# Kernel tuning notes

Hardware: AMD Instinct MI355X
Metric: run time of the kernel (lower is better)

## Reference

```python
import jax, jax.numpy as jnp
import numpy as np

N_SRC0, N_FTRS, N_HID, N_CLS = 200000, 128, 1500, 64
E0, E1 = 1600000, 500000
RES0, RES1 = 50000, 10000


def sage_conv(x, src, tgt, res_size, W_root, W_neigh, b):
    # mean aggregation of neighbor (source) features onto the first res_size target nodes
    msg = x[src]                                              # [E, F] gather
    summed = jax.ops.segment_sum(msg, tgt, num_segments=res_size)   # [res, F]
    cnt = jax.ops.segment_sum(jnp.ones((src.shape[0],), x.dtype), tgt, num_segments=res_size)
    mean = summed / jnp.maximum(cnt, 1.0)[:, None]
    return x[:res_size] @ W_root + mean @ W_neigh + b


def setup_inputs() -> dict:
    key = jax.random.key(0)
    ks = jax.random.split(key, 12)
    x = jax.random.normal(ks[0], (N_SRC0, N_FTRS), dtype=jnp.float32)
    edge_src0 = jax.random.randint(ks[1], (E0,), 0, N_SRC0)
    edge_tgt0 = jax.random.randint(ks[2], (E0,), 0, RES0)
    edge_src1 = jax.random.randint(ks[3], (E1,), 0, RES0)
    edge_tgt1 = jax.random.randint(ks[4], (E1,), 0, RES1)
    s1 = 1.0 / np.sqrt(N_FTRS)
    s2 = 1.0 / np.sqrt(N_HID)
    W1_root = jax.random.uniform(ks[5], (N_FTRS, N_HID), jnp.float32, -s1, s1)
    W1_neigh = jax.random.uniform(ks[6], (N_FTRS, N_HID), jnp.float32, -s1, s1)
    b1 = jax.random.uniform(ks[7], (N_HID,), jnp.float32, -s1, s1)
    W2_root = jax.random.uniform(ks[8], (N_HID, N_CLS), jnp.float32, -s2, s2)
    W2_neigh = jax.random.uniform(ks[9], (N_HID, N_CLS), jnp.float32, -s2, s2)
    b2 = jax.random.uniform(ks[10], (N_CLS,), jnp.float32, -s2, s2)
    return {
        "x": x,
        "W1_root": W1_root, "W1_neigh": W1_neigh, "b1": b1,
        "W2_root": W2_root, "W2_neigh": W2_neigh, "b2": b2,
        "edge_src0": edge_src0, "edge_tgt0": edge_tgt0,
        "edge_src1": edge_src1, "edge_tgt1": edge_tgt1,
        "res0": RES0, "res1": RES1,
    }


def reference(x, W1_root, W1_neigh, b1, W2_root, W2_neigh, b2,
              edge_src0, edge_tgt0, edge_src1, edge_tgt1, res0, res1):
    h = sage_conv(x, edge_src0, edge_tgt0, res0, W1_root, W1_neigh, b1)  # [res0, H]
    h = jax.nn.relu(h)
    # dropout p=0.5 is identity in eval mode
    out = sage_conv(h, edge_src1, edge_tgt1, res1, W2_root, W2_neigh, b2)  # [res1, C]
    return jax.nn.log_softmax(out, axis=1)
```

## Files before the change

### kernel.cpp

```cpp
#include <hip/hip_runtime.h>
#include <hip/hip_bf16.h>
#include <cstdint>
#include <cstddef>

#define NSRC   200000
#define NF     128
#define NHID   1500
#define NHIDP  1536
#define NCLS   64
#define E0N    1600000
#define E1N    500000
#define RES0   50000
#define RES1   10000

#define CH     4096
#define NCH0   ((E0N + CH - 1) / CH)
#define NCH1   ((E1N + CH - 1) / CH)
#define NB0    ((RES0 + 255) / 256)
#define NB1    ((RES1 + 255) / 256)

typedef __bf16 bf16x8 __attribute__((ext_vector_type(8)));
typedef float  f32x4  __attribute__((ext_vector_type(4)));
typedef unsigned short u16x8 __attribute__((ext_vector_type(8)));
typedef unsigned int u32;
typedef unsigned long long u64;

__device__ __forceinline__ unsigned short f2bf(float f) {
    union { float f; unsigned u; } v; v.f = f;
    unsigned r = v.u + 0x7fffu + ((v.u >> 16) & 1u);
    return (unsigned short)(r >> 16);
}

__device__ __forceinline__ void lds_dma16(const void* g, void* lds) {
    __builtin_amdgcn_global_load_lds(
        (const __attribute__((address_space(1))) unsigned int*)g,
        (__attribute__((address_space(3))) unsigned int*)lds, 16, 0, 0);
}

__global__ void prep_kernel(const float* __restrict__ W1r, const float* __restrict__ W1n,
                            const float* __restrict__ b1,
                            const float* __restrict__ W2r, const float* __restrict__ W2n,
                            unsigned short* __restrict__ WcatT,
                            unsigned short* __restrict__ W2catT,
                            float* __restrict__ b1e) {
    int id = blockIdx.x * 256 + threadIdx.x;
    if (id < 256 * NHIDP) {
        int n = id >> 8, k = id & 255;
        float v = 0.f;
        if (n < NHID) v = (k < NF) ? W1r[k * NHID + n] : W1n[(k - NF) * NHID + n];
        WcatT[n * 256 + k] = f2bf(v);
    } else {
        int id2 = id - 256 * NHIDP;
        if (id2 < 128 * NHIDP) {
            int n = id2 / NHIDP, k = id2 % NHIDP;
            float v = 0.f;
            if (k < NHID) v = (n < 64) ? W2n[k * 64 + n] : W2r[k * 64 + (n - 64)];
            W2catT[n * NHIDP + k] = f2bf(v);
        } else {
            int c = id2 - 128 * NHIDP;
            if (c < NHIDP) b1e[c] = (c < NHID) ? b1[c] : 0.f;
        }
    }
}

__global__ __launch_bounds__(256) void copyx_kernel(const float* __restrict__ x,
                                                    unsigned short* __restrict__ xbf) {
    size_t i = ((size_t)blockIdx.x * 256 + threadIdx.x) * 8;
    const float4* s = (const float4*)(x + i);
    float4 a = s[0], b = s[1];
    u16x8 o;
    o[0] = f2bf(a.x); o[1] = f2bf(a.y); o[2] = f2bf(a.z); o[3] = f2bf(a.w);
    o[4] = f2bf(b.x); o[5] = f2bf(b.y); o[6] = f2bf(b.z); o[7] = f2bf(b.w);
    *(u16x8*)(xbf + i) = o;
}

__global__ __launch_bounds__(256) void p1a_kernel(const int* __restrict__ tgt, int n,
                                                  int nb, u32* __restrict__ H) {
    __shared__ u32 lhist[256];
    int c = blockIdx.x, tid = threadIdx.x;
    lhist[tid] = 0;
    __syncthreads();
#pragma unroll
    for (int it = 0; it < CH / 256; ++it) {
        int i = c * CH + it * 256 + tid;
        if (i < n) atomicAdd(&lhist[((u32)tgt[i]) >> 8], 1u);
    }
    __syncthreads();
    if (tid < nb) H[c * nb + tid] = lhist[tid];
}

__global__ __launch_bounds__(512) void bscan_kernel(const u32* __restrict__ H,
                                                    int nch, int nb,
                                                    u32* __restrict__ base_rel,
                                                    u32* __restrict__ Bsum) {
    __shared__ u32 part[512];
    int b = blockIdx.x, t = threadIdx.x;
    part[t] = (t < nch) ? H[t * nb + b] : 0u;
    __syncthreads();
    for (int d = 1; d < 512; d <<= 1) {
        u32 v = part[t];
        u32 add = (t >= d) ? part[t - d] : 0u;
        __syncthreads();
        part[t] = v + add;
        __syncthreads();
    }
    if (t < nch) base_rel[t * nb + b] = (t == 0) ? 0u : part[t - 1];
    if (t == 0) Bsum[b] = part[nch - 1];
}

__global__ __launch_bounds__(256) void boff_kernel(const u32* __restrict__ Bsum1,
                                                   u32* __restrict__ boff1, int nb1,
                                                   const u32* __restrict__ Bsum2,
                                                   u32* __restrict__ boff2, int nb2) {
    const u32* B = blockIdx.x ? Bsum2 : Bsum1;
    u32* O = blockIdx.x ? boff2 : boff1;
    int nb = blockIdx.x ? nb2 : nb1;
    __shared__ u32 part[256];
    int t = threadIdx.x;
    part[t] = (t < nb) ? B[t] : 0u;
    __syncthreads();
    for (int d = 1; d < 256; d <<= 1) {
        u32 v = part[t];
        u32 add = (t >= d) ? part[t - d] : 0u;
        __syncthreads();
        part[t] = v + add;
        __syncthreads();
    }
    if (t < nb) O[t] = (t == 0) ? 0u : part[t - 1];
}

__global__ __launch_bounds__(256) void p1b_kernel(const int* __restrict__ src,
                                                  const int* __restrict__ tgt, int n,
                                                  int nb, const u32* __restrict__ base_rel,
                                                  const u32* __restrict__ boff,
                                                  u64* __restrict__ bucketed) {
    __shared__ u32 lcur[256];
    __shared__ u32 lbase[256];
    int c = blockIdx.x, tid = threadIdx.x;
    lcur[tid] = 0;
    if (tid < nb) lbase[tid] = base_rel[c * nb + tid] + boff[tid];
    __syncthreads();
#pragma unroll
    for (int it = 0; it < CH / 256; ++it) {
        int i = c * CH + it * 256 + tid;
        if (i < n) {
            u32 t = (u32)tgt[i];
            u32 s = (u32)src[i];
            u32 b = t >> 8;
            u32 r = atomicAdd(&lcur[b], 1u);
            bucketed[lbase[b] + r] = ((u64)t << 32) | (u64)s;
        }
    }
}

__global__ __launch_bounds__(1024) void p2_kernel(const u64* __restrict__ bucketed,
                                                  const u32* __restrict__ boff,
                                                  int nb, int res, int etot,
                                                  int* __restrict__ csr,
                                                  u32* __restrict__ off_out,
                                                  u32* __restrict__ cnt_out) {
    __shared__ u32 lhist[256];
    __shared__ u32 part[256];
    __shared__ u32 cur[256];
    int b = blockIdx.x, tid = threadIdx.x;
    u32 start = boff[b];
    u32 end = (b == nb - 1) ? (u32)etot : boff[b + 1];
    u32 count = end - start;
    if (tid < 256) lhist[tid] = 0;
    __syncthreads();
    for (u32 i = tid; i < count; i += 1024) {
        u32 t = (u32)(bucketed[start + i] >> 32);
        atomicAdd(&lhist[t & 255u], 1u);
    }
    __syncthreads();
    if (tid < 256) part[tid] = lhist[tid];
    __syncthreads();
    for (int d = 1; d < 256; d <<= 1) {
        u32 v = (tid < 256) ? part[tid] : 0u;
        u32 add = (tid >= d && tid < 256) ? part[tid - d] : 0u;
        __syncthreads();
        if (tid < 256) part[tid] = v + add;
        __syncthreads();
    }
    if (tid < 256) {
        u32 excl = (tid == 0) ? 0u : part[tid - 1];
        cur[tid] = excl;
        int tg = (b << 8) + tid;
        if (tg < res) {
            off_out[tg] = start + excl;
            cnt_out[tg] = lhist[tid];
        }
    }
    __syncthreads();
    for (u32 i = tid; i < count; i += 1024) {
        u64 pr = bucketed[start + i];
        u32 lt = ((u32)(pr >> 32)) & 255u;
        u32 r = atomicAdd(&cur[lt], 1u);
        csr[start + r] = (int)(u32)pr;
    }
}

__global__ __launch_bounds__(256) void agg1_csr_kernel(
        const u32* __restrict__ xb32, const int* __restrict__ csr,
        const u32* __restrict__ off, const u32* __restrict__ cnt,
        u32* __restrict__ mean1_32) {
    int row = blockIdx.x * 4 + (threadIdx.x >> 6);
    int lane = threadIdx.x & 63;
    if (row >= RES0) return;
    u32 base = off[row], deg = cnt[row];
    float x0 = 0.f, y0 = 0.f, x1 = 0.f, y1 = 0.f;
    float x2 = 0.f, y2 = 0.f, x3 = 0.f, y3 = 0.f;
    u32 e = 0;
    for (; e + 4 <= deg; e += 4) {
        int s0 = csr[base + e], s1 = csr[base + e + 1];
        int s2 = csr[base + e + 2], s3 = csr[base + e + 3];
        u32 w0 = xb32[(size_t)s0 * 64 + lane];
        u32 w1 = xb32[(size_t)s1 * 64 + lane];
        u32 w2 = xb32[(size_t)s2 * 64 + lane];
        u32 w3 = xb32[(size_t)s3 * 64 + lane];
        union { u32 u; float f; } a, b;
        a.u = w0 << 16; b.u = w0 & 0xffff0000u; x0 += a.f; y0 += b.f;
        a.u = w1 << 16; b.u = w1 & 0xffff0000u; x1 += a.f; y1 += b.f;
        a.u = w2 << 16; b.u = w2 & 0xffff0000u; x2 += a.f; y2 += b.f;
        a.u = w3 << 16; b.u = w3 & 0xffff0000u; x3 += a.f; y3 += b.f;
    }
    for (; e < deg; ++e) {
        u32 w = xb32[(size_t)csr[base + e] * 64 + lane];
        union { u32 u; float f; } a, b;
        a.u = w << 16; b.u = w & 0xffff0000u; x0 += a.f; y0 += b.f;
    }
    float inv = 1.0f / fmaxf((float)deg, 1.0f);
    float mx = ((x0 + x1) + (x2 + x3)) * inv;
    float my = ((y0 + y1) + (y2 + y3)) * inv;
    mean1_32[(size_t)row * 64 + lane] = (u32)f2bf(mx) | ((u32)f2bf(my) << 16);
}

__global__ __launch_bounds__(256, 2) void fused_gemm_kernel(
        const unsigned short* __restrict__ xbf, const unsigned short* __restrict__ mean1,
        const unsigned short* __restrict__ WcatT, const float* __restrict__ b1e,
        const unsigned short* __restrict__ W2catT,
        float* __restrict__ pp0, float* __restrict__ pp1) {
    __shared__ __align__(16) unsigned short As[128 * 32];
    __shared__ __align__(16) unsigned short Bs[128 * 32];
    __shared__ __align__(16) unsigned short Ht[128 * 136];

    int m0 = blockIdx.x * 128;
    int jb = blockIdx.y * 6;
    float* pout = blockIdx.y ? pp1 : pp0;
    int tid = threadIdx.x;
    int lane = tid & 63, wid = tid >> 6;
    int wm = wid >> 1, wn = wid & 1;
    int quad = lane >> 4, l15 = lane & 15;

    f32x4 pacc[4][4] = {};

    for (int j = jb; j < jb + 6; ++j) {
        f32x4 hacc[4][4] = {};
        for (int kk = 0; kk < 256; kk += 32) {
#pragma unroll
            for (int ci = 0; ci < 2; ++ci) {
                int cb = ci * 256 + wid * 64;
                int chunk = cb + lane;
                int n = chunk >> 2, kc = chunk & 3;
                const unsigned short* g = (kk < 128)
                    ? xbf + (size_t)(m0 + n) * NF + kk + kc * 8
                    : mean1 + (size_t)(m0 + n) * NF + (kk - 128) + kc * 8;
                lds_dma16(g, &As[cb * 8]);
            }
#pragma unroll
            for (int ci = 0; ci < 2; ++ci) {
                int cb = ci * 256 + wid * 64;
                int chunk = cb + lane;
                int n = chunk >> 2, kc = chunk & 3;
                const unsigned short* g = WcatT + (size_t)(j * 128 + n) * 256 + kk + kc * 8;
                lds_dma16(g, &Bs[cb * 8]);
            }
            __syncthreads();
            bf16x8 a[4], b[4];
#pragma unroll
            for (int mi = 0; mi < 4; ++mi)
                a[mi] = *(const bf16x8*)(&As[(wm * 64 + mi * 16 + l15) * 32 + quad * 8]);
#pragma unroll
            for (int ni = 0; ni < 4; ++ni)
                b[ni] = *(const bf16x8*)(&Bs[(wn * 64 + ni * 16 + l15) * 32 + quad * 8]);
#pragma unroll
            for (int mi = 0; mi < 4; ++mi)
#pragma unroll
                for (int ni = 0; ni < 4; ++ni)
                    hacc[mi][ni] = __builtin_amdgcn_mfma_f32_16x16x32_bf16(a[mi], b[ni], hacc[mi][ni], 0, 0, 0);
            __syncthreads();
        }
#pragma unroll
        for (int ni = 0; ni < 4; ++ni) {
            int lc = wn * 64 + ni * 16 + l15;
            float bv = b1e[j * 128 + lc];
#pragma unroll
            for (int mi = 0; mi < 4; ++mi) {
#pragma unroll
                for (int r = 0; r < 4; ++r) {
                    int row = wm * 64 + mi * 16 + quad * 4 + r;
                    Ht[row * 136 + lc] = f2bf(fmaxf(hacc[mi][ni][r] + bv, 0.f));
                }
            }
        }
        __syncthreads();
#pragma unroll
        for (int kk2 = 0; kk2 < 128; kk2 += 32) {
            bf16x8 a2[4], b2[4];
#pragma unroll
            for (int mi = 0; mi < 4; ++mi)
                a2[mi] = *(const bf16x8*)(&Ht[(wm * 64 + mi * 16 + l15) * 136 + kk2 + quad * 8]);
#pragma unroll
            for (int ni = 0; ni < 4; ++ni)
                b2[ni] = *(const bf16x8*)(W2catT + (size_t)(wn * 64 + ni * 16 + l15) * NHIDP
                                          + j * 128 + kk2 + quad * 8);
#pragma unroll
            for (int mi = 0; mi < 4; ++mi)
#pragma unroll
                for (int ni = 0; ni < 4; ++ni)
                    pacc[mi][ni] = __builtin_amdgcn_mfma_f32_16x16x32_bf16(a2[mi], b2[ni], pacc[mi][ni], 0, 0, 0);
        }
        __syncthreads();
    }

#pragma unroll
    for (int ni = 0; ni < 4; ++ni) {
        int gc = wn * 64 + ni * 16 + l15;
#pragma unroll
        for (int mi = 0; mi < 4; ++mi) {
#pragma unroll
            for (int r = 0; r < 4; ++r) {
                int gr = m0 + wm * 64 + mi * 16 + quad * 4 + r;
                if (gr < RES0) pout[(size_t)gr * 128 + gc] = pacc[mi][ni][r];
            }
        }
    }
}

__global__ __launch_bounds__(256) void padd_kernel(float* __restrict__ pp0,
                                                   const float* __restrict__ pp1) {
    size_t i = (size_t)blockIdx.x * 256 + threadIdx.x;
    f32x4 a = ((const f32x4*)pp0)[i];
    f32x4 b = ((const f32x4*)pp1)[i];
    ((f32x4*)pp0)[i] = a + b;
}

__global__ __launch_bounds__(64) void final_csr_kernel(
        const float* __restrict__ p, const int* __restrict__ csr,
        const u32* __restrict__ off, const u32* __restrict__ cnt,
        const float* __restrict__ b2, float* __restrict__ out) {
    int row = blockIdx.x;
    int c = threadIdx.x;
    u32 base = off[row], deg = cnt[row];
    float a0 = 0.f, a1 = 0.f, a2 = 0.f, a3 = 0.f;
    u32 e = 0;
    for (; e + 4 <= deg; e += 4) {
        int s0 = csr[base + e], s1 = csr[base + e + 1];
        int s2 = csr[base + e + 2], s3 = csr[base + e + 3];
        a0 += p[(size_t)s0 * 128 + c];
        a1 += p[(size_t)s1 * 128 + c];
        a2 += p[(size_t)s2 * 128 + c];
        a3 += p[(size_t)s3 * 128 + c];
    }
    for (; e < deg; ++e) a0 += p[(size_t)csr[base + e] * 128 + c];
    float mean = ((a0 + a1) + (a2 + a3)) / fmaxf((float)deg, 1.0f);
    float v = p[(size_t)row * 128 + 64 + c] + mean + b2[c];
    float m = v;
#pragma unroll
    for (int o = 32; o > 0; o >>= 1) m = fmaxf(m, __shfl_xor(m, o, 64));
    float ex = expf(v - m);
    float s = ex;
#pragma unroll
    for (int o = 32; o > 0; o >>= 1) s += __shfl_xor(s, o, 64);
    out[(size_t)row * 64 + c] = v - m - logf(s);
}

extern "C" void kernel_launch(void* const* d_in, const int* in_sizes, int n_in,
                              void* d_out, int out_size, void* d_ws, size_t ws_size,
                              hipStream_t stream) {
    const float* x   = (const float*)d_in[0];
    const float* W1r = (const float*)d_in[1];
    const float* W1n = (const float*)d_in[2];
    const float* b1  = (const float*)d_in[3];
    const float* W2r = (const float*)d_in[4];
    const float* W2n = (const float*)d_in[5];
    const float* b2  = (const float*)d_in[6];
    const int* es0 = (const int*)d_in[7];
    const int* et0 = (const int*)d_in[8];
    const int* es1 = (const int*)d_in[9];
    const int* et1 = (const int*)d_in[10];
    float* out = (float*)d_out;

    char* ws = (char*)d_ws;
    const size_t PPBYTES = (size_t)RES0 * 128 * 4;
    float* pp1 = (float*)ws;
    size_t o0 = 0;
    auto alloc0 = [&](size_t bytes) {
        void* ptr = ws + o0;
        o0 = (o0 + bytes + 255) & ~(size_t)255;
        return ptr;
    };
    u64* bkt1  = (u64*)alloc0((size_t)E0N * 8);
    u64* bkt2  = (u64*)alloc0((size_t)E1N * 8);
    int* csr1  = (int*)alloc0((size_t)E0N * 4);
    u32* H1    = (u32*)alloc0((size_t)NCH0 * NB0 * 4);
    u32* base1 = (u32*)alloc0((size_t)NCH0 * NB0 * 4);
    u32* H2    = (u32*)alloc0((size_t)NCH1 * NB1 * 4);
    u32* base2 = (u32*)alloc0((size_t)NCH1 * NB1 * 4);
    u32* Bsum1 = (u32*)alloc0((size_t)NB0 * 4);
    u32* Bsum2 = (u32*)alloc0((size_t)NB1 * 4);
    u32* boff1 = (u32*)alloc0((size_t)NB0 * 4);
    u32* boff2 = (u32*)alloc0((size_t)NB1 * 4);
    u32* off1  = (u32*)alloc0((size_t)RES0 * 4);
    u32* cnt1  = (u32*)alloc0((size_t)RES0 * 4);

    size_t off_ = PPBYTES;
    auto alloc = [&](size_t bytes) {
        void* ptr = ws + off_;
        off_ = (off_ + bytes + 255) & ~(size_t)255;
        return ptr;
    };
    int* csr2  = (int*)alloc((size_t)E1N * 4);
    u32* off2  = (u32*)alloc((size_t)RES1 * 4);
    u32* cnt2  = (u32*)alloc((size_t)RES1 * 4);
    unsigned short* xbf    = (unsigned short*)alloc((size_t)NSRC * NF * 2);
    unsigned short* mean1  = (unsigned short*)alloc((size_t)(RES0 + 128) * NF * 2);
    unsigned short* WcatT  = (unsigned short*)alloc((size_t)NHIDP * 256 * 2);
    unsigned short* W2catT = (unsigned short*)alloc((size_t)128 * NHIDP * 2);
    float*          b1e    = (float*)alloc((size_t)NHIDP * 4);
    float*          pp0    = (float*)alloc(PPBYTES);

    prep_kernel<<<(256 * NHIDP + 128 * NHIDP + NHIDP + 255) / 256, 256, 0, stream>>>(
        W1r, W1n, b1, W2r, W2n, WcatT, W2catT, b1e);

    copyx_kernel<<<(NSRC * NF) / (256 * 8), 256, 0, stream>>>(x, xbf);

    p1a_kernel<<<NCH0, 256, 0, stream>>>(et0, E0N, NB0, H1);
    p1a_kernel<<<NCH1, 256, 0, stream>>>(et1, E1N, NB1, H2);
    bscan_kernel<<<NB0, 512, 0, stream>>>(H1, NCH0, NB0, base1, Bsum1);
    bscan_kernel<<<NB1, 512, 0, stream>>>(H2, NCH1, NB1, base2, Bsum2);
    boff_kernel<<<2, 256, 0, stream>>>(Bsum1, boff1, NB0, Bsum2, boff2, NB1);
    p1b_kernel<<<NCH0, 256, 0, stream>>>(es0, et0, E0N, NB0, base1, boff1, bkt1);
    p1b_kernel<<<NCH1, 256, 0, stream>>>(es1, et1, E1N, NB1, base2, boff2, bkt2);
    p2_kernel<<<NB0, 1024, 0, stream>>>(bkt1, boff1, NB0, RES0, E0N, csr1, off1, cnt1);
    p2_kernel<<<NB1, 1024, 0, stream>>>(bkt2, boff2, NB1, RES1, E1N, csr2, off2, cnt2);

    agg1_csr_kernel<<<(RES0 + 3) / 4, 256, 0, stream>>>(
        (const u32*)xbf, csr1, off1, cnt1, (u32*)mean1);

    fused_gemm_kernel<<<dim3((RES0 + 127) / 128, 2), 256, 0, stream>>>(
        xbf, mean1, WcatT, b1e, W2catT, pp0, pp1);

    padd_kernel<<<(RES0 * 128 / 4 + 255) / 256, 256, 0, stream>>>(pp0, pp1);

    final_csr_kernel<<<RES1, 64, 0, stream>>>(pp0, csr2, off2, cnt2, b2, out);
}
```

Baseline: 499.5 us.

## Merge paired preprocessing launches and load two K-slices per GEMM barrier

Result: faster. 460.8 us (-7.8%).

```diff
diff --git a/kernel.cpp b/kernel.cpp
--- a/kernel.cpp
+++ b/kernel.cpp
@@ -19,6 +19,9 @@
 #define NB0    ((RES0 + 255) / 256)
 #define NB1    ((RES1 + 255) / 256)
 
+#define PREP_BLOCKS  ((256 * NHIDP + 128 * NHIDP + NHIDP + 255) / 256)
+#define COPYX_BLOCKS ((NSRC * NF) / (256 * 8))
+
 typedef __bf16 bf16x8 __attribute__((ext_vector_type(8)));
 typedef float  f32x4  __attribute__((ext_vector_type(4)));
 typedef unsigned short u16x8 __attribute__((ext_vector_type(8)));
@@ -37,47 +40,48 @@
         (__attribute__((address_space(3))) unsigned int*)lds, 16, 0, 0);
 }
 
-__global__ void prep_kernel(const float* __restrict__ W1r, const float* __restrict__ W1n,
-                            const float* __restrict__ b1,
-                            const float* __restrict__ W2r, const float* __restrict__ W2n,
-                            unsigned short* __restrict__ WcatT,
-                            unsigned short* __restrict__ W2catT,
-                            float* __restrict__ b1e) {
-    int id = blockIdx.x * 256 + threadIdx.x;
-    if (id < 256 * NHIDP) {
-        int n = id >> 8, k = id & 255;
-        float v = 0.f;
-        if (n < NHID) v = (k < NF) ? W1r[k * NHID + n] : W1n[(k - NF) * NHID + n];
-        WcatT[n * 256 + k] = f2bf(v);
+__global__ __launch_bounds__(256) void setup_kernel(
+        const float* __restrict__ x, unsigned short* __restrict__ xbf,
+        const float* __restrict__ W1r, const float* __restrict__ W1n,
+        const float* __restrict__ b1,
+        const float* __restrict__ W2r, const float* __restrict__ W2n,
+        unsigned short* __restrict__ WcatT, unsigned short* __restrict__ W2catT,
+        float* __restrict__ b1e) {
+    int bid = blockIdx.x;
+    if (bid < PREP_BLOCKS) {
+        int id = bid * 256 + threadIdx.x;
+        if (id < 256 * NHIDP) {
+            int n = id >> 8, k = id & 255;
+            float v = 0.f;
+            if (n < NHID) v = (k < NF) ? W1r[k * NHID + n] : W1n[(k - NF) * NHID + n];
+            WcatT[n * 256 + k] = f2bf(v);
+        } else {
+            int id2 = id - 256 * NHIDP;
+            if (id2 < 128 * NHIDP) {
+                int n = id2 / NHIDP, k = id2 % NHIDP;
+                float v = 0.f;
+                if (k < NHID) v = (n < 64) ? W2n[k * 64 + n] : W2r[k * 64 + (n - 64)];
+                W2catT[n * NHIDP + k] = f2bf(v);
+            } else {
+                int c = id2 - 128 * NHIDP;
+                if (c < NHIDP) b1e[c] = (c < NHID) ? b1[c] : 0.f;
+            }
+        }
     } else {
-        int id2 = id - 256 * NHIDP;
-        if (id2 < 128 * NHIDP) {
-            int n = id2 / NHIDP, k = id2 % NHIDP;
-            float v = 0.f;
-            if (k < NHID) v = (n < 64) ? W2n[k * 64 + n] : W2r[k * 64 + (n - 64)];
-            W2catT[n * NHIDP + k] = f2bf(v);
-        } else {
-            int c = id2 - 128 * NHIDP;
-            if (c < NHIDP) b1e[c] = (c < NHID) ? b1[c] : 0.f;
-        }
-    }
-}
-
-__global__ __launch_bounds__(256) void copyx_kernel(const float* __restrict__ x,
-                                                    unsigned short* __restrict__ xbf) {
-    size_t i = ((size_t)blockIdx.x * 256 + threadIdx.x) * 8;
-    const float4* s = (const float4*)(x + i);
-    float4 a = s[0], b = s[1];
-    u16x8 o;
-    o[0] = f2bf(a.x); o[1] = f2bf(a.y); o[2] = f2bf(a.z); o[3] = f2bf(a.w);
-    o[4] = f2bf(b.x); o[5] = f2bf(b.y); o[6] = f2bf(b.z); o[7] = f2bf(b.w);
-    *(u16x8*)(xbf + i) = o;
-}
-
-__global__ __launch_bounds__(256) void p1a_kernel(const int* __restrict__ tgt, int n,
-                                                  int nb, u32* __restrict__ H) {
+        size_t i = ((size_t)(bid - PREP_BLOCKS) * 256 + threadIdx.x) * 8;
+        const float4* s = (const float4*)(x + i);
+        float4 a = s[0], b = s[1];
+        u16x8 o;
+        o[0] = f2bf(a.x); o[1] = f2bf(a.y); o[2] = f2bf(a.z); o[3] = f2bf(a.w);
+        o[4] = f2bf(b.x); o[5] = f2bf(b.y); o[6] = f2bf(b.z); o[7] = f2bf(b.w);
+        *(u16x8*)(xbf + i) = o;
+    }
+}
+
+__device__ __forceinline__ void p1a_body(const int* __restrict__ tgt, int n,
+                                         int nb, u32* __restrict__ H, int c) {
     __shared__ u32 lhist[256];
-    int c = blockIdx.x, tid = threadIdx.x;
+    int tid = threadIdx.x;
     lhist[tid] = 0;
     __syncthreads();
 #pragma unroll
@@ -89,12 +93,20 @@
     if (tid < nb) H[c * nb + tid] = lhist[tid];
 }
 
-__global__ __launch_bounds__(512) void bscan_kernel(const u32* __restrict__ H,
-                                                    int nch, int nb,
-                                                    u32* __restrict__ base_rel,
-                                                    u32* __restrict__ Bsum) {
+__global__ __launch_bounds__(256) void p1a_both_kernel(
+        const int* __restrict__ t0, const int* __restrict__ t1,
+        u32* __restrict__ H1, u32* __restrict__ H2) {
+    int b = blockIdx.x;
+    if (b < NCH0) p1a_body(t0, E0N, NB0, H1, b);
+    else          p1a_body(t1, E1N, NB1, H2, b - NCH0);
+}
+
+__device__ __forceinline__ void bscan_body(const u32* __restrict__ H,
+                                           int nch, int nb, int b,
+                                           u32* __restrict__ base_rel,
+                                           u32* __restrict__ Bsum) {
     __shared__ u32 part[512];
-    int b = blockIdx.x, t = threadIdx.x;
+    int t = threadIdx.x;
     part[t] = (t < nch) ? H[t * nb + b] : 0u;
     __syncthreads();
     for (int d = 1; d < 512; d <<= 1) {
@@ -106,6 +118,14 @@
     }
     if (t < nch) base_rel[t * nb + b] = (t == 0) ? 0u : part[t - 1];
     if (t == 0) Bsum[b] = part[nch - 1];
+}
+
+__global__ __launch_bounds__(512) void bscan_both_kernel(
+        const u32* __restrict__ H1, u32* __restrict__ base1, u32* __restrict__ Bsum1,
+        const u32* __restrict__ H2, u32* __restrict__ base2, u32* __restrict__ Bsum2) {
+    int b = blockIdx.x;
+    if (b < NB0) bscan_body(H1, NCH0, NB0, b, base1, Bsum1);
+    else         bscan_body(H2, NCH1, NB1, b - NB0, base2, Bsum2);
 }
 
 __global__ __launch_bounds__(256) void boff_kernel(const u32* __restrict__ Bsum1,
@@ -129,14 +149,14 @@
     if (t < nb) O[t] = (t == 0) ? 0u : part[t - 1];
 }
 
-__global__ __launch_bounds__(256) void p1b_kernel(const int* __restrict__ src,
-                                                  const int* __restrict__ tgt, int n,
-                                                  int nb, const u32* __restrict__ base_rel,
-                                                  const u32* __restrict__ boff,
-                                                  u64* __restrict__ bucketed) {
+__device__ __forceinline__ void p1b_body(const int* __restrict__ src,
+                                         const int* __restrict__ tgt, int n,
+                                         int nb, const u32* __restrict__ base_rel,
+                                         const u32* __restrict__ boff,
+                                         u64* __restrict__ bucketed, int c) {
     __shared__ u32 lcur[256];
     __shared__ u32 lbase[256];
-    int c = blockIdx.x, tid = threadIdx.x;
+    int tid = threadIdx.x;
     lcur[tid] = 0;
     if (tid < nb) lbase[tid] = base_rel[c * nb + tid] + boff[tid];
     __syncthreads();
@@ -153,16 +173,28 @@
     }
 }
 
-__global__ __launch_bounds__(1024) void p2_kernel(const u64* __restrict__ bucketed,
-                                                  const u32* __restrict__ boff,
-                                                  int nb, int res, int etot,
-                                                  int* __restrict__ csr,
-                                                  u32* __restrict__ off_out,
-                                                  u32* __restrict__ cnt_out) {
+__global__ __launch_bounds__(256) void p1b_both_kernel(
+        const int* __restrict__ s0, const int* __restrict__ t0,
+        const u32* __restrict__ base1, const u32* __restrict__ boff1,
+        u64* __restrict__ bkt1,
+        const int* __restrict__ s1, const int* __restrict__ t1,
+        const u32* __restrict__ base2, const u32* __restrict__ boff2,
+        u64* __restrict__ bkt2) {
+    int b = blockIdx.x;
+    if (b < NCH0) p1b_body(s0, t0, E0N, NB0, base1, boff1, bkt1, b);
+    else          p1b_body(s1, t1, E1N, NB1, base2, boff2, bkt2, b - NCH0);
+}
+
+__device__ __forceinline__ void p2_body(const u64* __restrict__ bucketed,
+                                        const u32* __restrict__ boff,
+                                        int nb, int res, int etot,
+                                        int* __restrict__ csr,
+                                        u32* __restrict__ off_out,
+                                        u32* __restrict__ cnt_out, int b) {
     __shared__ u32 lhist[256];
     __shared__ u32 part[256];
     __shared__ u32 cur[256];
-    int b = blockIdx.x, tid = threadIdx.x;
+    int tid = threadIdx.x;
     u32 start = boff[b];
     u32 end = (b == nb - 1) ? (u32)etot : boff[b + 1];
     u32 count = end - start;
@@ -198,6 +230,16 @@
         u32 r = atomicAdd(&cur[lt], 1u);
         csr[start + r] = (int)(u32)pr;
     }
+}
+
+__global__ __launch_bounds__(1024) void p2_both_kernel(
+        const u64* __restrict__ bkt1, const u32* __restrict__ boff1,
+        int* __restrict__ csr1, u32* __restrict__ off1, u32* __restrict__ cnt1,
+        const u64* __restrict__ bkt2, const u32* __restrict__ boff2,
+        int* __restrict__ csr2, u32* __restrict__ off2, u32* __restrict__ cnt2) {
+    int b = blockIdx.x;
+    if (b < NB0) p2_body(bkt1, boff1, NB0, RES0, E0N, csr1, off1, cnt1, b);
+    else         p2_body(bkt2, boff2, NB1, RES1, E1N, csr2, off2, cnt2, b - NB0);
 }
 
 __global__ __launch_bounds__(256) void agg1_csr_kernel(
@@ -240,8 +282,10 @@
         const unsigned short* __restrict__ WcatT, const float* __restrict__ b1e,
         const unsigned short* __restrict__ W2catT,
         float* __restrict__ pp0, float* __restrict__ pp1) {
-    __shared__ __align__(16) unsigned short As[128 * 32];
-    __shared__ __align__(16) unsigned short Bs[128 * 32];
+    __shared__ __align__(16) unsigned short As0[128 * 32];
+    __shared__ __align__(16) unsigned short As1[128 * 32];
+    __shared__ __align__(16) unsigned short Bs0[128 * 32];
+    __shared__ __align__(16) unsigned short Bs1[128 * 32];
     __shared__ __align__(16) unsigned short Ht[128 * 136];
 
     int m0 = blockIdx.x * 128;
@@ -256,38 +300,53 @@
 
     for (int j = jb; j < jb + 6; ++j) {
         f32x4 hacc[4][4] = {};
-        for (int kk = 0; kk < 256; kk += 32) {
-#pragma unroll
-            for (int ci = 0; ci < 2; ++ci) {
-                int cb = ci * 256 + wid * 64;
-                int chunk = cb + lane;
-                int n = chunk >> 2, kc = chunk & 3;
-                const unsigned short* g = (kk < 128)
-                    ? xbf + (size_t)(m0 + n) * NF + kk + kc * 8
-                    : mean1 + (size_t)(m0 + n) * NF + (kk - 128) + kc * 8;
-                lds_dma16(g, &As[cb * 8]);
+        for (int kk = 0; kk < 256; kk += 64) {
+#pragma unroll
+            for (int kh = 0; kh < 2; ++kh) {
+                int ksel = kk + kh * 32;
+                const unsigned short* src = (ksel < 128)
+                    ? xbf + (size_t)m0 * NF + ksel
+                    : mean1 + (size_t)m0 * NF + (ksel - 128);
+                unsigned short* dst = kh ? As1 : As0;
+#pragma unroll
+                for (int ci = 0; ci < 2; ++ci) {
+                    int cb = ci * 256 + wid * 64;
+                    int chunk = cb + lane;
+                    int n = chunk >> 2, kc = chunk & 3;
+                    lds_dma16(src + (size_t)n * NF + kc * 8, &dst[cb * 8]);
+                }
             }
 #pragma unroll
-            for (int ci = 0; ci < 2; ++ci) {
-                int cb = ci * 256 + wid * 64;
-                int chunk = cb + lane;
-                int n = chunk >> 2, kc = chunk & 3;
-                const unsigned short* g = WcatT + (size_t)(j * 128 + n) * 256 + kk + kc * 8;
-                lds_dma16(g, &Bs[cb * 8]);
+            for (int kh = 0; kh < 2; ++kh) {
+                int ksel = kk + kh * 32;
+                const unsigned short* src = WcatT + (size_t)(j * 128) * 256 + ksel;
+                unsigned short* dst = kh ? Bs1 : Bs0;
+#pragma unroll
+                for (int ci = 0; ci < 2; ++ci) {
+                    int cb = ci * 256 + wid * 64;
+                    int chunk = cb + lane;
+                    int n = chunk >> 2, kc = chunk & 3;
+                    lds_dma16(src + (size_t)n * 256 + kc * 8, &dst[cb * 8]);
+                }
             }
             __syncthreads();
-            bf16x8 a[4], b[4];
-#pragma unroll
-            for (int mi = 0; mi < 4; ++mi)
-                a[mi] = *(const bf16x8*)(&As[(wm * 64 + mi * 16 + l15) * 32 + quad * 8]);
-#pragma unroll
-            for (int ni = 0; ni < 4; ++ni)
-                b[ni] = *(const bf16x8*)(&Bs[(wn * 64 + ni * 16 + l15) * 32 + quad * 8]);
-#pragma unroll
-            for (int mi = 0; mi < 4; ++mi)
+#pragma unroll
+            for (int kh = 0; kh < 2; ++kh) {
+                const unsigned short* Asb = kh ? As1 : As0;
+                const unsigned short* Bsb = kh ? Bs1 : Bs0;
+                bf16x8 a[4], b[4];
+#pragma unroll
+                for (int mi = 0; mi < 4; ++mi)
+                    a[mi] = *(const bf16x8*)(&Asb[(wm * 64 + mi * 16 + l15) * 32 + quad * 8]);
 #pragma unroll
                 for (int ni = 0; ni < 4; ++ni)
-                    hacc[mi][ni] = __builtin_amdgcn_mfma_f32_16x16x32_bf16(a[mi], b[ni], hacc[mi][ni], 0, 0, 0);
+                    b[ni] = *(const bf16x8*)(&Bsb[(wn * 64 + ni * 16 + l15) * 32 + quad * 8]);
+#pragma unroll
+                for (int mi = 0; mi < 4; ++mi)
+#pragma unroll
+                    for (int ni = 0; ni < 4; ++ni)
+                        hacc[mi][ni] = __builtin_amdgcn_mfma_f32_16x16x32_bf16(a[mi], b[ni], hacc[mi][ni], 0, 0, 0);
+            }
             __syncthreads();
         }
 #pragma unroll
@@ -430,20 +489,16 @@
     float*          b1e    = (float*)alloc((size_t)NHIDP * 4);
     float*          pp0    = (float*)alloc(PPBYTES);
 
-    prep_kernel<<<(256 * NHIDP + 128 * NHIDP + NHIDP + 255) / 256, 256, 0, stream>>>(
-        W1r, W1n, b1, W2r, W2n, WcatT, W2catT, b1e);
-
-    copyx_kernel<<<(NSRC * NF) / (256 * 8), 256, 0, stream>>>(x, xbf);
-
-    p1a_kernel<<<NCH0, 256, 0, stream>>>(et0, E0N, NB0, H1);
-    p1a_kernel<<<NCH1, 256, 0, stream>>>(et1, E1N, NB1, H2);
-    bscan_kernel<<<NB0, 512, 0, stream>>>(H1, NCH0, NB0, base1, Bsum1);
-    bscan_kernel<<<NB1, 512, 0, stream>>>(H2, NCH1, NB1, base2, Bsum2);
+    setup_kernel<<<PREP_BLOCKS + COPYX_BLOCKS, 256, 0, stream>>>(
+        x, xbf, W1r, W1n, b1, W2r, W2n, WcatT, W2catT, b1e);
+
+    p1a_both_kernel<<<NCH0 + NCH1, 256, 0, stream>>>(et0, et1, H1, H2);
+    bscan_both_kernel<<<NB0 + NB1, 512, 0, stream>>>(H1, base1, Bsum1, H2, base2, Bsum2);
     boff_kernel<<<2, 256, 0, stream>>>(Bsum1, boff1, NB0, Bsum2, boff2, NB1);
-    p1b_kernel<<<NCH0, 256, 0, stream>>>(es0, et0, E0N, NB0, base1, boff1, bkt1);
-    p1b_kernel<<<NCH1, 256, 0, stream>>>(es1, et1, E1N, NB1, base2, boff2, bkt2);
-    p2_kernel<<<NB0, 1024, 0, stream>>>(bkt1, boff1, NB0, RES0, E0N, csr1, off1, cnt1);
-    p2_kernel<<<NB1, 1024, 0, stream>>>(bkt2, boff2, NB1, RES1, E1N, csr2, off2, cnt2);
+    p1b_both_kernel<<<NCH0 + NCH1, 256, 0, stream>>>(
+        es0, et0, base1, boff1, bkt1, es1, et1, base2, boff2, bkt2);
+    p2_both_kernel<<<NB0 + NB1, 1024, 0, stream>>>(
+        bkt1, boff1, csr1, off1, cnt1, bkt2, boff2, csr2, off2, cnt2);
 
     agg1_csr_kernel<<<(RES0 + 3) / 4, 256, 0, stream>>>(
         (const u32*)xbf, csr1, off1, cnt1, (u32*)mean1);
```
